# Optimization experiments

Hardware: AMD Instinct MI355X
Metric: run time of the kernel (lower is better)

Reference implementation:

```python
import jax, jax.numpy as jnp
import numpy as np

EPSILON = 0.1
NSTEPS = 2
SIGN = 1.0  # forward integration (sample direction)


def setup_inputs() -> dict:
    key = jax.random.key(0)
    ks = jax.random.split(key, 6)
    B, D, H = 4096, 32, 256
    x = jax.random.normal(ks[0], (B, D), jnp.float32)
    logp = jax.random.normal(ks[1], (B,), jnp.float32)
    w1 = jax.random.normal(ks[2], (D, H), jnp.float32) / np.sqrt(D).astype(np.float32)
    b1 = jax.random.normal(ks[3], (H,), jnp.float32) * 0.01
    w2 = jax.random.normal(ks[4], (H,), jnp.float32) / np.sqrt(H).astype(np.float32)
    b2 = jax.random.normal(ks[5], (1,), jnp.float32) * 0.01
    return {"x": x, "logp": logp, "w1": w1, "b1": b1, "w2": w2, "b2": b2}


def reference(x, logp, w1, b1, w2, b2):
    D = x.shape[-1]

    def u(xi):  # scalar Brenier potential for a single sample [D] -> scalar
        h = jax.nn.softplus(xi @ w1 + b1)
        return h @ w2 + b2[0]

    grad_u = jax.grad(u)  # net.grad: du/dx, [D] -> [D]

    def lap_u(xi):  # net.laplacian: trace of Hessian via forward-over-reverse HVPs
        eye = jnp.eye(D, dtype=xi.dtype)
        hvp = lambda v: jax.jvp(grad_u, (xi,), (v,))[1]
        return jnp.trace(jax.vmap(hvp)(eye))

    v_grad = jax.vmap(grad_u)   # [B,D] -> [B,D]
    v_lap = jax.vmap(lap_u)     # [B,D] -> [B]

    def ode(xc):
        return SIGN * EPSILON * v_grad(xc), -SIGN * EPSILON * v_lap(xc)

    def step(carry, _):
        xc, lp = carry
        k1x, k1l = ode(xc)
        k2x, k2l = ode(xc + k1x / 2)
        k3x, k3l = ode(xc + k2x / 2)
        k4x, k4l = ode(xc + k3x)
        xc = xc + (k1x / 6.0 + k2x / 3.0 + k3x / 3.0 + k4x / 6.0)
        lp = lp + (k1l / 6.0 + k2l / 3.0 + k3l / 3.0 + k4l / 6.0)
        return (xc, lp), None

    (x, logp), _ = jax.lax.scan(step, (x, logp), None, length=NSTEPS)
    return x, logp
```

## Files before the change

### kernel.cpp

```cpp
#include <hip/hip_runtime.h>

#define B_TOTAL 4096
#define D 32
#define H 256
#define SPB 16
#define NW 8
#define HPW 32

static constexpr float EPS = 0.1f;

typedef __attribute__((ext_vector_type(8))) short short8v;
typedef __attribute__((ext_vector_type(4))) float f32x4;

__device__ __forceinline__ unsigned short bf16rne(float f) {
  unsigned u = __float_as_uint(f);
  u += 0x7FFFu + ((u >> 16) & 1u);
  return (unsigned short)(u >> 16);
}
__device__ __forceinline__ float fromb(unsigned short h) {
  return __uint_as_float(((unsigned)h) << 16);
}
__device__ __forceinline__ void split_rne(float f, unsigned short& hi, unsigned short& lo) {
  hi = bf16rne(f); lo = bf16rne(f - fromb(hi));
}

#define MFMA16(A, Bf, C) __builtin_amdgcn_mfma_f32_16x16x32_bf16((A), (Bf), (C), 0, 0, 0)

__global__ __launch_bounds__(512, 2) void ma_flow_kernel(
    const float* __restrict__ x_in, const float* __restrict__ logp_in,
    const float* __restrict__ w1, const float* __restrict__ b1,
    const float* __restrict__ w2, float* __restrict__ out)
{
  __shared__ __align__(16) unsigned aBuf[NW][SPB][36];
  __shared__ __align__(16) float partG[NW][SPB][36];
  __shared__ __align__(16) float xcL[SPB][36];

  const int tid = threadIdx.x;
  const int l  = tid & 63;
  const int wv = tid >> 6;
  const int lr = l & 15;
  const int lg = l >> 4;
  const int hbase = wv * HPW;
  const int s_own = tid >> 5;
  const int d_own = tid & 31;

  short8v Bzh[2], Bzl[2];
  float b1v[2], w2v[2], w2cv[2];
#pragma unroll
  for (int tau = 0; tau < 2; ++tau) {
    const int h = hbase + tau * 16 + lr;
    float cpart = 0.0f;
    short8v hi, lo;
#pragma unroll
    for (int j = 0; j < 8; ++j) {
      float w = w1[(lg * 8 + j) * H + h];
      cpart = fmaf(w, w, cpart);
      unsigned short hb, lb; split_rne(w, hb, lb);
      hi[j] = (short)hb; lo[j] = (short)lb;
    }
    Bzh[tau] = hi; Bzl[tau] = lo;
    cpart += __shfl_xor(cpart, 16);
    cpart += __shfl_xor(cpart, 32);
    b1v[tau] = b1[h];
    float w2x = w2[h];
    w2v[tau] = w2x;
    w2cv[tau] = w2x * cpart;
  }
  short8v Bgh[2], Bgl[2];
#pragma unroll
  for (int nu = 0; nu < 2; ++nu) {
    const int d = nu * 16 + lr;
    const float* pp = w1 + d * H + hbase + lg * 8;
    float4 v0 = *reinterpret_cast<const float4*>(pp);
    float4 v1 = *reinterpret_cast<const float4*>(pp + 4);
    float wv8[8] = {v0.x, v0.y, v0.z, v0.w, v1.x, v1.y, v1.z, v1.w};
    short8v hi, lo;
#pragma unroll
    for (int j = 0; j < 8; ++j) {
      unsigned short hb, lb; split_rne(wv8[j], hb, lb);
      hi[j] = (short)hb; lo[j] = (short)lb;
    }
    Bgh[nu] = hi; Bgl[nu] = lo;
  }

  float x0r = x_in[blockIdx.x * (SPB * D) + tid];
  float accr = 0.0f;
  xcL[s_own][d_own] = x0r;
  float lp = (tid < SPB) ? logp_in[blockIdx.x * SPB + tid] : 0.0f;
  float lapAcc[4] = {0.0f, 0.0f, 0.0f, 0.0f};
  __syncthreads();

#pragma unroll 1
  for (int stage = 0; stage < 8; ++stage) {
    const int st = stage & 3;
    const float wa = (st == 0 || st == 3) ? (EPS / 6.0f) : (EPS / 3.0f);
    const float wc = (st == 2) ? EPS : (EPS * 0.5f);

    const float* xrow = &xcL[lr][lg * 8];
    f32x4 xv0 = *reinterpret_cast<const f32x4*>(xrow);
    f32x4 xv1 = *reinterpret_cast<const f32x4*>(xrow + 4);
    short8v ahi, alo;
#pragma unroll
    for (int j = 0; j < 4; ++j) {
      float xa = xv0[j];
      unsigned u = __float_as_uint(xa);
      ahi[j] = (short)(u >> 16);
      alo[j] = (short)(__float_as_uint(xa - __uint_as_float(u & 0xFFFF0000u)) >> 16);
      float xb = xv1[j];
      unsigned u2 = __float_as_uint(xb);
      ahi[4 + j] = (short)(u2 >> 16);
      alo[4 + j] = (short)(__float_as_uint(xb - __uint_as_float(u2 & 0xFFFF0000u)) >> 16);
    }

    float slap[4] = {0.0f, 0.0f, 0.0f, 0.0f};
#pragma unroll
    for (int tau = 0; tau < 2; ++tau) {
      f32x4 z = {b1v[tau], b1v[tau], b1v[tau], b1v[tau]};
      z = MFMA16(ahi, Bzh[tau], z);
      z = MFMA16(alo, Bzh[tau], z);
      z = MFMA16(ahi, Bzl[tau], z);
#pragma unroll
      for (int r = 0; r < 4; ++r) {
        float E = __expf(-z[r]);
        float t = __builtin_amdgcn_rcpf(1.0f + E);
        float a = t * w2v[tau];
        slap[r] = fmaf(t * t * E, w2cv[tau], slap[r]);
        unsigned ua = __float_as_uint(a);
        float fh = __uint_as_float(ua & 0xFFFF0000u);
        unsigned ul = __float_as_uint(a - fh);
        unsigned* bp = &aBuf[wv][lg * 4 + r][lr];
        bp[tau * 16] = (ul & 0xFFFF0000u) | (ua >> 16);
      }
    }
#pragma unroll
    for (int r = 0; r < 4; ++r) lapAcc[r] = fmaf(wa, slap[r], lapAcc[r]);

    asm volatile("s_waitcnt lgkmcnt(0)" ::: "memory");
    __builtin_amdgcn_sched_barrier(0);

    const unsigned* ap = &aBuf[wv][lr][lg * 8];
    uint4 q0 = *reinterpret_cast<const uint4*>(ap);
    uint4 q1 = *reinterpret_cast<const uint4*>(ap + 4);
    unsigned uu[8] = {q0.x, q0.y, q0.z, q0.w, q1.x, q1.y, q1.z, q1.w};
    short8v aH, aL;
#pragma unroll
    for (int j = 0; j < 8; ++j) {
      aH[j] = (short)(uu[j] & 0xFFFFu);
      aL[j] = (short)(uu[j] >> 16);
    }
#pragma unroll
    for (int nu = 0; nu < 2; ++nu) {
      f32x4 g = {0.0f, 0.0f, 0.0f, 0.0f};
      g = MFMA16(aH, Bgh[nu], g);
      g = MFMA16(aL, Bgh[nu], g);
      g = MFMA16(aH, Bgl[nu], g);
#pragma unroll
      for (int r = 0; r < 4; ++r)
        partG[wv][lg * 4 + r][nu * 16 + lr] = g[r];
    }
    __syncthreads();

    float gsum = 0.0f;
#pragma unroll
    for (int w = 0; w < NW; ++w) gsum += partG[w][s_own][d_own];
    accr = fmaf(wa, gsum, accr);
    float xw;
    if (st < 3) {
      xw = fmaf(wc, gsum, x0r);
    } else {
      x0r += accr; accr = 0.0f; xw = x0r;
    }
    xcL[s_own][d_own] = xw;
    __syncthreads();
  }

#pragma unroll
  for (int m = 1; m < 16; m <<= 1)
#pragma unroll
    for (int r = 0; r < 4; ++r) lapAcc[r] += __shfl_xor(lapAcc[r], m);
  if (lr == 0) {
#pragma unroll
    for (int r = 0; r < 4; ++r) partG[wv][lg * 4 + r][0] = lapAcc[r];
  }
  __syncthreads();

  out[blockIdx.x * (SPB * D) + tid] = x0r;
  if (tid < SPB) {
    float lt = 0.0f;
#pragma unroll
    for (int w = 0; w < NW; ++w) lt += partG[w][tid][0];
    out[B_TOTAL * D + blockIdx.x * SPB + tid] = lp - lt;
  }
}

extern "C" void kernel_launch(void* const* d_in, const int* in_sizes, int n_in,
                              void* d_out, int out_size, void* d_ws, size_t ws_size,
                              hipStream_t stream) {
  const float* x    = (const float*)d_in[0];
  const float* logp = (const float*)d_in[1];
  const float* w1   = (const float*)d_in[2];
  const float* b1   = (const float*)d_in[3];
  const float* w2   = (const float*)d_in[4];
  float* out = (float*)d_out;

  ma_flow_kernel<<<B_TOTAL / SPB, 512, 0, stream>>>(x, logp, w1, b1, w2, out);
}
```

Before: 16.25 us.

## Pre-split x into packed bf16 pairs and vectorize LDS stores via permuted hidden layout

The writer of each x update now stores a packed hi/lo bf16 pair in shared memory, so readers no longer split it per stage. The hidden-unit order inside each wave is permuted so the activation and partial-gradient writes become 8-byte vector stores, with the w1 gradient fragments loaded in the matching order. Each 3-MFMA chain is split into two independent accumulators to shorten the dependency chain, and the partial-gradient reduction is now a tree sum. It also drops a scheduling barrier, which trades strided scalar w1 loads at setup for fewer LDS instructions in the loop.

```diff
diff --git a/kernel.cpp b/kernel.cpp
--- a/kernel.cpp
+++ b/kernel.cpp
@@ -6,6 +6,7 @@
 #define SPB 16
 #define NW 8
 #define HPW 32
+#define PGS 34
 
 static constexpr float EPS = 0.1f;
 
@@ -22,6 +23,11 @@
 }
 __device__ __forceinline__ void split_rne(float f, unsigned short& hi, unsigned short& lo) {
   hi = bf16rne(f); lo = bf16rne(f - fromb(hi));
+}
+__device__ __forceinline__ unsigned packsplit(float a) {
+  unsigned ua = __float_as_uint(a);
+  float fh = __uint_as_float(ua & 0xFFFF0000u);
+  return (ua & 0xFFFF0000u) | (__float_as_uint(a - fh) >> 16);
 }
 
 #define MFMA16(A, Bf, C) __builtin_amdgcn_mfma_f32_16x16x32_bf16((A), (Bf), (C), 0, 0, 0)
@@ -32,8 +38,8 @@
     const float* __restrict__ w2, float* __restrict__ out)
 {
   __shared__ __align__(16) unsigned aBuf[NW][SPB][36];
-  __shared__ __align__(16) float partG[NW][SPB][36];
-  __shared__ __align__(16) float xcL[SPB][36];
+  __shared__ __align__(16) float partG[NW][SPB][PGS];
+  __shared__ __align__(16) unsigned xcP[SPB][36];
 
   const int tid = threadIdx.x;
   const int l  = tid & 63;
@@ -43,6 +49,7 @@
   const int hbase = wv * HPW;
   const int s_own = tid >> 5;
   const int d_own = tid & 31;
+  const int posd = ((d_own & 15) << 1) | (d_own >> 4);
 
   short8v Bzh[2], Bzl[2];
   float b1v[2], w2v[2], w2cv[2];
@@ -70,14 +77,13 @@
 #pragma unroll
   for (int nu = 0; nu < 2; ++nu) {
     const int d = nu * 16 + lr;
-    const float* pp = w1 + d * H + hbase + lg * 8;
-    float4 v0 = *reinterpret_cast<const float4*>(pp);
-    float4 v1 = *reinterpret_cast<const float4*>(pp + 4);
-    float wv8[8] = {v0.x, v0.y, v0.z, v0.w, v1.x, v1.y, v1.z, v1.w};
     short8v hi, lo;
 #pragma unroll
     for (int j = 0; j < 8; ++j) {
-      unsigned short hb, lb; split_rne(wv8[j], hb, lb);
+      const int p = lg * 8 + j;
+      const int h = hbase + ((p & 1) << 4) + (p >> 1);
+      float w = w1[d * H + h];
+      unsigned short hb, lb; split_rne(w, hb, lb);
       hi[j] = (short)hb; lo[j] = (short)lb;
     }
     Bgh[nu] = hi; Bgl[nu] = lo;
@@ -85,7 +91,7 @@
 
   float x0r = x_in[blockIdx.x * (SPB * D) + tid];
   float accr = 0.0f;
-  xcL[s_own][d_own] = x0r;
+  xcP[s_own][d_own] = packsplit(x0r);
   float lp = (tid < SPB) ? logp_in[blockIdx.x * SPB + tid] : 0.0f;
   float lapAcc[4] = {0.0f, 0.0f, 0.0f, 0.0f};
   __syncthreads();
@@ -96,47 +102,40 @@
     const float wa = (st == 0 || st == 3) ? (EPS / 6.0f) : (EPS / 3.0f);
     const float wc = (st == 2) ? EPS : (EPS * 0.5f);
 
-    const float* xrow = &xcL[lr][lg * 8];
-    f32x4 xv0 = *reinterpret_cast<const f32x4*>(xrow);
-    f32x4 xv1 = *reinterpret_cast<const f32x4*>(xrow + 4);
+    const unsigned* xp = &xcP[lr][lg * 8];
+    uint4 xq0 = *reinterpret_cast<const uint4*>(xp);
+    uint4 xq1 = *reinterpret_cast<const uint4*>(xp + 4);
+    unsigned xu[8] = {xq0.x, xq0.y, xq0.z, xq0.w, xq1.x, xq1.y, xq1.z, xq1.w};
     short8v ahi, alo;
 #pragma unroll
-    for (int j = 0; j < 4; ++j) {
-      float xa = xv0[j];
-      unsigned u = __float_as_uint(xa);
-      ahi[j] = (short)(u >> 16);
-      alo[j] = (short)(__float_as_uint(xa - __uint_as_float(u & 0xFFFF0000u)) >> 16);
-      float xb = xv1[j];
-      unsigned u2 = __float_as_uint(xb);
-      ahi[4 + j] = (short)(u2 >> 16);
-      alo[4 + j] = (short)(__float_as_uint(xb - __uint_as_float(u2 & 0xFFFF0000u)) >> 16);
-    }
-
-    float slap[4] = {0.0f, 0.0f, 0.0f, 0.0f};
+    for (int j = 0; j < 8; ++j) {
+      ahi[j] = (short)(xu[j] >> 16);
+      alo[j] = (short)(xu[j] & 0xFFFFu);
+    }
+
+    f32x4 zz[2];
 #pragma unroll
     for (int tau = 0; tau < 2; ++tau) {
-      f32x4 z = {b1v[tau], b1v[tau], b1v[tau], b1v[tau]};
-      z = MFMA16(ahi, Bzh[tau], z);
-      z = MFMA16(alo, Bzh[tau], z);
-      z = MFMA16(ahi, Bzl[tau], z);
-#pragma unroll
-      for (int r = 0; r < 4; ++r) {
-        float E = __expf(-z[r]);
-        float t = __builtin_amdgcn_rcpf(1.0f + E);
-        float a = t * w2v[tau];
-        slap[r] = fmaf(t * t * E, w2cv[tau], slap[r]);
-        unsigned ua = __float_as_uint(a);
-        float fh = __uint_as_float(ua & 0xFFFF0000u);
-        unsigned ul = __float_as_uint(a - fh);
-        unsigned* bp = &aBuf[wv][lg * 4 + r][lr];
-        bp[tau * 16] = (ul & 0xFFFF0000u) | (ua >> 16);
-      }
-    }
-#pragma unroll
-    for (int r = 0; r < 4; ++r) lapAcc[r] = fmaf(wa, slap[r], lapAcc[r]);
+      f32x4 zA = {b1v[tau], b1v[tau], b1v[tau], b1v[tau]};
+      f32x4 zB = {0.0f, 0.0f, 0.0f, 0.0f};
+      zA = MFMA16(ahi, Bzh[tau], zA);
+      zB = MFMA16(ahi, Bzl[tau], zB);
+      zB = MFMA16(alo, Bzh[tau], zB);
+      zz[tau] = zA + zB;
+    }
+#pragma unroll
+    for (int r = 0; r < 4; ++r) {
+      float E0 = __expf(-zz[0][r]);
+      float t0 = __builtin_amdgcn_rcpf(1.0f + E0);
+      float E1 = __expf(-zz[1][r]);
+      float t1 = __builtin_amdgcn_rcpf(1.0f + E1);
+      float q = fmaf(t1 * t1 * E1, w2cv[1], (t0 * t0 * E0) * w2cv[0]);
+      lapAcc[r] = fmaf(wa, q, lapAcc[r]);
+      *reinterpret_cast<uint2*>(&aBuf[wv][lg * 4 + r][2 * lr]) =
+          make_uint2(packsplit(t0 * w2v[0]), packsplit(t1 * w2v[1]));
+    }
 
     asm volatile("s_waitcnt lgkmcnt(0)" ::: "memory");
-    __builtin_amdgcn_sched_barrier(0);
 
     const unsigned* ap = &aBuf[wv][lr][lg * 8];
     uint4 q0 = *reinterpret_cast<const uint4*>(ap);
@@ -145,24 +144,31 @@
     short8v aH, aL;
 #pragma unroll
     for (int j = 0; j < 8; ++j) {
-      aH[j] = (short)(uu[j] & 0xFFFFu);
-      aL[j] = (short)(uu[j] >> 16);
-    }
+      aH[j] = (short)(uu[j] >> 16);
+      aL[j] = (short)(uu[j] & 0xFFFFu);
+    }
+    f32x4 gg[2];
 #pragma unroll
     for (int nu = 0; nu < 2; ++nu) {
-      f32x4 g = {0.0f, 0.0f, 0.0f, 0.0f};
-      g = MFMA16(aH, Bgh[nu], g);
-      g = MFMA16(aL, Bgh[nu], g);
-      g = MFMA16(aH, Bgl[nu], g);
-#pragma unroll
-      for (int r = 0; r < 4; ++r)
-        partG[wv][lg * 4 + r][nu * 16 + lr] = g[r];
+      f32x4 gA = {0.0f, 0.0f, 0.0f, 0.0f};
+      f32x4 gB = {0.0f, 0.0f, 0.0f, 0.0f};
+      gA = MFMA16(aH, Bgh[nu], gA);
+      gB = MFMA16(aH, Bgl[nu], gB);
+      gB = MFMA16(aL, Bgh[nu], gB);
+      gg[nu] = gA + gB;
+    }
+#pragma unroll
+    for (int r = 0; r < 4; ++r) {
+      *reinterpret_cast<float2*>(&partG[wv][lg * 4 + r][2 * lr]) =
+          make_float2(gg[0][r], gg[1][r]);
     }
     __syncthreads();
 
-    float gsum = 0.0f;
-#pragma unroll
-    for (int w = 0; w < NW; ++w) gsum += partG[w][s_own][d_own];
+    float p0 = partG[0][s_own][posd], p1 = partG[1][s_own][posd];
+    float p2 = partG[2][s_own][posd], p3 = partG[3][s_own][posd];
+    float p4 = partG[4][s_own][posd], p5 = partG[5][s_own][posd];
+    float p6 = partG[6][s_own][posd], p7 = partG[7][s_own][posd];
+    float gsum = ((p0 + p1) + (p2 + p3)) + ((p4 + p5) + (p6 + p7));
     accr = fmaf(wa, gsum, accr);
     float xw;
     if (st < 3) {
@@ -170,7 +176,7 @@
     } else {
       x0r += accr; accr = 0.0f; xw = x0r;
     }
-    xcL[s_own][d_own] = xw;
+    xcP[s_own][d_own] = packsplit(xw);
     __syncthreads();
   }
 
```

Result: slower. 17.01 us (+4.6%).

## Pre-split x into bf16 hi/lo in LDS and drop third MFMA in gradient

Applied to the files above, without the earlier changes.

The producer thread now splits each state value into bf16 hi/lo halves once, storing them in LDS with a permuted K-index layout, so each wave loads ready-made MFMA operands instead of reconverting fp32. The softplus-derivative activations are rounded to a single bf16 rather than split into hi/lo, which cuts the gradient GEMM from three MFMAs to two per tile and halves the aBuf footprint. W1 is loaded with a matching permutation, the two tau tiles' activations are computed together, and the partial-gradient reduction becomes a tree. This removes conversion ALU work and one MFMA pass, at the cost of lower precision in the gradient path and scalar instead of vector W1 loads at setup.

```diff
diff --git a/kernel.cpp b/kernel.cpp
--- a/kernel.cpp
+++ b/kernel.cpp
@@ -6,6 +6,9 @@
 #define SPB 16
 #define NW 8
 #define HPW 32
+#define ABS 20
+#define PGS 36
+#define XCS 40
 
 static constexpr float EPS = 0.1f;
 
@@ -25,15 +28,17 @@
 }
 
 #define MFMA16(A, Bf, C) __builtin_amdgcn_mfma_f32_16x16x32_bf16((A), (Bf), (C), 0, 0, 0)
+
 
 __global__ __launch_bounds__(512, 2) void ma_flow_kernel(
     const float* __restrict__ x_in, const float* __restrict__ logp_in,
     const float* __restrict__ w1, const float* __restrict__ b1,
     const float* __restrict__ w2, float* __restrict__ out)
 {
-  __shared__ __align__(16) unsigned aBuf[NW][SPB][36];
-  __shared__ __align__(16) float partG[NW][SPB][36];
-  __shared__ __align__(16) float xcL[SPB][36];
+  __shared__ __align__(16) unsigned aBuf[NW][SPB][ABS];
+  __shared__ __align__(16) float partG[NW][SPB][PGS];
+  __shared__ __align__(16) unsigned short xcH[SPB][XCS];
+  __shared__ __align__(16) unsigned short xcL[SPB][XCS];
 
   const int tid = threadIdx.x;
   const int l  = tid & 63;
@@ -43,6 +48,7 @@
   const int hbase = wv * HPW;
   const int s_own = tid >> 5;
   const int d_own = tid & 31;
+  const int xci = ((d_own & 15) << 1) | (d_own >> 4);
 
   short8v Bzh[2], Bzl[2];
   float b1v[2], w2v[2], w2cv[2];
@@ -53,7 +59,8 @@
     short8v hi, lo;
 #pragma unroll
     for (int j = 0; j < 8; ++j) {
-      float w = w1[(lg * 8 + j) * H + h];
+      const int dj = lg * 4 + (j >> 1) + ((j & 1) << 4);
+      float w = w1[dj * H + h];
       cpart = fmaf(w, w, cpart);
       unsigned short hb, lb; split_rne(w, hb, lb);
       hi[j] = (short)hb; lo[j] = (short)lb;
@@ -70,14 +77,12 @@
 #pragma unroll
   for (int nu = 0; nu < 2; ++nu) {
     const int d = nu * 16 + lr;
-    const float* pp = w1 + d * H + hbase + lg * 8;
-    float4 v0 = *reinterpret_cast<const float4*>(pp);
-    float4 v1 = *reinterpret_cast<const float4*>(pp + 4);
-    float wv8[8] = {v0.x, v0.y, v0.z, v0.w, v1.x, v1.y, v1.z, v1.w};
     short8v hi, lo;
 #pragma unroll
     for (int j = 0; j < 8; ++j) {
-      unsigned short hb, lb; split_rne(wv8[j], hb, lb);
+      const int hl = lg * 4 + (j >> 1) + ((j & 1) << 4);
+      float w = w1[d * H + hbase + hl];
+      unsigned short hb, lb; split_rne(w, hb, lb);
       hi[j] = (short)hb; lo[j] = (short)lb;
     }
     Bgh[nu] = hi; Bgl[nu] = lo;
@@ -85,7 +90,12 @@
 
   float x0r = x_in[blockIdx.x * (SPB * D) + tid];
   float accr = 0.0f;
-  xcL[s_own][d_own] = x0r;
+  {
+    unsigned u = __float_as_uint(x0r);
+    xcH[s_own][xci] = (unsigned short)(u >> 16);
+    float res = x0r - __uint_as_float(u & 0xFFFF0000u);
+    xcL[s_own][xci] = (unsigned short)(__float_as_uint(res) >> 16);
+  }
   float lp = (tid < SPB) ? logp_in[blockIdx.x * SPB + tid] : 0.0f;
   float lapAcc[4] = {0.0f, 0.0f, 0.0f, 0.0f};
   __syncthreads();
@@ -96,73 +106,51 @@
     const float wa = (st == 0 || st == 3) ? (EPS / 6.0f) : (EPS / 3.0f);
     const float wc = (st == 2) ? EPS : (EPS * 0.5f);
 
-    const float* xrow = &xcL[lr][lg * 8];
-    f32x4 xv0 = *reinterpret_cast<const f32x4*>(xrow);
-    f32x4 xv1 = *reinterpret_cast<const f32x4*>(xrow + 4);
-    short8v ahi, alo;
-#pragma unroll
-    for (int j = 0; j < 4; ++j) {
-      float xa = xv0[j];
-      unsigned u = __float_as_uint(xa);
-      ahi[j] = (short)(u >> 16);
-      alo[j] = (short)(__float_as_uint(xa - __uint_as_float(u & 0xFFFF0000u)) >> 16);
-      float xb = xv1[j];
-      unsigned u2 = __float_as_uint(xb);
-      ahi[4 + j] = (short)(u2 >> 16);
-      alo[4 + j] = (short)(__float_as_uint(xb - __uint_as_float(u2 & 0xFFFF0000u)) >> 16);
-    }
-
-    float slap[4] = {0.0f, 0.0f, 0.0f, 0.0f};
+    short8v ahi = *reinterpret_cast<const short8v*>(&xcH[lr][lg * 8]);
+    short8v alo = *reinterpret_cast<const short8v*>(&xcL[lr][lg * 8]);
+
+    f32x4 zz[2];
 #pragma unroll
     for (int tau = 0; tau < 2; ++tau) {
       f32x4 z = {b1v[tau], b1v[tau], b1v[tau], b1v[tau]};
       z = MFMA16(ahi, Bzh[tau], z);
       z = MFMA16(alo, Bzh[tau], z);
       z = MFMA16(ahi, Bzl[tau], z);
-#pragma unroll
-      for (int r = 0; r < 4; ++r) {
-        float E = __expf(-z[r]);
-        float t = __builtin_amdgcn_rcpf(1.0f + E);
-        float a = t * w2v[tau];
-        slap[r] = fmaf(t * t * E, w2cv[tau], slap[r]);
-        unsigned ua = __float_as_uint(a);
-        float fh = __uint_as_float(ua & 0xFFFF0000u);
-        unsigned ul = __float_as_uint(a - fh);
-        unsigned* bp = &aBuf[wv][lg * 4 + r][lr];
-        bp[tau * 16] = (ul & 0xFFFF0000u) | (ua >> 16);
-      }
-    }
-#pragma unroll
-    for (int r = 0; r < 4; ++r) lapAcc[r] = fmaf(wa, slap[r], lapAcc[r]);
+      zz[tau] = z;
+    }
+#pragma unroll
+    for (int r = 0; r < 4; ++r) {
+      float E0 = __expf(-zz[0][r]);
+      float t0 = __builtin_amdgcn_rcpf(1.0f + E0);
+      float E1 = __expf(-zz[1][r]);
+      float t1 = __builtin_amdgcn_rcpf(1.0f + E1);
+      float q = fmaf(t1 * t1 * E1, w2cv[1], (t0 * t0 * E0) * w2cv[0]);
+      lapAcc[r] = fmaf(wa, q, lapAcc[r]);
+      aBuf[wv][lg * 4 + r][lr] =
+          (unsigned)bf16rne(t0 * w2v[0]) | ((unsigned)bf16rne(t1 * w2v[1]) << 16);
+    }
 
     asm volatile("s_waitcnt lgkmcnt(0)" ::: "memory");
     __builtin_amdgcn_sched_barrier(0);
 
-    const unsigned* ap = &aBuf[wv][lr][lg * 8];
-    uint4 q0 = *reinterpret_cast<const uint4*>(ap);
-    uint4 q1 = *reinterpret_cast<const uint4*>(ap + 4);
-    unsigned uu[8] = {q0.x, q0.y, q0.z, q0.w, q1.x, q1.y, q1.z, q1.w};
-    short8v aH, aL;
-#pragma unroll
-    for (int j = 0; j < 8; ++j) {
-      aH[j] = (short)(uu[j] & 0xFFFFu);
-      aL[j] = (short)(uu[j] >> 16);
-    }
+    uint4 aq = *reinterpret_cast<const uint4*>(&aBuf[wv][lr][lg * 4]);
+    short8v aF = *reinterpret_cast<const short8v*>(&aq);
 #pragma unroll
     for (int nu = 0; nu < 2; ++nu) {
       f32x4 g = {0.0f, 0.0f, 0.0f, 0.0f};
-      g = MFMA16(aH, Bgh[nu], g);
-      g = MFMA16(aL, Bgh[nu], g);
-      g = MFMA16(aH, Bgl[nu], g);
+      g = MFMA16(aF, Bgh[nu], g);
+      g = MFMA16(aF, Bgl[nu], g);
 #pragma unroll
       for (int r = 0; r < 4; ++r)
         partG[wv][lg * 4 + r][nu * 16 + lr] = g[r];
     }
     __syncthreads();
 
-    float gsum = 0.0f;
-#pragma unroll
-    for (int w = 0; w < NW; ++w) gsum += partG[w][s_own][d_own];
+    float p0 = partG[0][s_own][d_own], p1 = partG[1][s_own][d_own];
+    float p2 = partG[2][s_own][d_own], p3 = partG[3][s_own][d_own];
+    float p4 = partG[4][s_own][d_own], p5 = partG[5][s_own][d_own];
+    float p6 = partG[6][s_own][d_own], p7 = partG[7][s_own][d_own];
+    float gsum = ((p0 + p1) + (p2 + p3)) + ((p4 + p5) + (p6 + p7));
     accr = fmaf(wa, gsum, accr);
     float xw;
     if (st < 3) {
@@ -170,7 +158,12 @@
     } else {
       x0r += accr; accr = 0.0f; xw = x0r;
     }
-    xcL[s_own][d_own] = xw;
+    {
+      unsigned u = __float_as_uint(xw);
+      xcH[s_own][xci] = (unsigned short)(u >> 16);
+      float res = xw - __uint_as_float(u & 0xFFFF0000u);
+      xcL[s_own][xci] = (unsigned short)(__float_as_uint(res) >> 16);
+    }
     __syncthreads();
   }
 
```

Measured after the change: 15.26 us. -6.1%, faster.
